# Kernel tuning notes

Hardware: AMD Instinct MI355X
Metric: run time of the kernel (lower is better)

## Reference

```python
import jax, jax.numpy as jnp
import numpy as np

H = 128            # hidden_channels
HM = 2 * H         # _inner_mlp_mult * H
N = 50000          # num nodes
E = 400000         # num edges
M = 800000         # num node-edge incidences (2 per edge)
BN_EPS = 1e-5


def _bn_relu(x, g, b):
    # BatchNorm1d in training mode: population stats over the batch dim, then affine + ReLU
    m = x.mean(0)
    v = ((x - m) ** 2).mean(0)
    return jax.nn.relu((x - m) * jax.lax.rsqrt(v + BN_EPS) * g + b)


def setup_inputs() -> dict:
    key = jax.random.key(0)
    ks = jax.random.split(key, 12)
    node_rep = jax.random.normal(ks[0], (N, H), dtype=jnp.float32)
    edge_rep = jax.random.normal(ks[1], (E, H), dtype=jnp.float32)
    src = jax.random.randint(ks[2], (M,), 0, N, dtype=jnp.int32)
    dst = jax.random.randint(ks[3], (M,), 0, E, dtype=jnp.int32)
    node2edge_index = jnp.stack([src, dst], 0)

    def lin(k, fan_in, fan_out):
        return jax.random.normal(k, (fan_in, fan_out), dtype=jnp.float32) / np.sqrt(fan_in)

    return {
        "node_rep": node_rep,
        "edge_rep": edge_rep,
        "node2edge_index": node2edge_index,
        # lvl_mlp_1: Linear(2H->H, no bias), BN(H), ReLU
        "Wa": lin(ks[4], 2 * H, H), "ga": jnp.ones((H,)), "ba": jnp.zeros((H,)),
        # lvl_mlp_2: Linear(H->2H), BN, ReLU, Linear(2H->H), BN, ReLU
        "Wb1": lin(ks[5], H, HM), "gb1": jnp.ones((HM,)), "bb1": jnp.zeros((HM,)),
        "Wb2": lin(ks[6], HM, H), "gb2": jnp.ones((H,)), "bb2": jnp.zeros((H,)),
        # lift_mlp: Linear(H->2H), BN, ReLU, Linear(2H->H), BN, ReLU
        "Wl1": lin(ks[7], H, HM), "gl1": jnp.ones((HM,)), "bl1": jnp.zeros((HM,)),
        "Wl2": lin(ks[8], HM, H), "gl2": jnp.ones((H,)), "bl2": jnp.zeros((H,)),
        "eps1": jnp.zeros(()), "eps2": jnp.zeros(()),
    }


def reference(node_rep, edge_rep, node2edge_index,
              Wa, ga, ba,
              Wb1, gb1, bb1, Wb2, gb2, bb2,
              Wl1, gl1, bl1, Wl2, gl2, bl2,
              eps1, eps2):
    src = node2edge_index[0]  # node index per incidence
    dst = node2edge_index[1]  # edge index per incidence

    # node -> edge gather + scatter_sum
    node2edge_val = node_rep[src]                                   # [M, H]
    lift_aggr = jax.ops.segment_sum(node2edge_val, dst, num_segments=E)  # [E, H]

    # lvl_mlp_1 on concatenated edge features
    lvl_aggr_edge = _bn_relu(jnp.concatenate([lift_aggr, edge_rep], -1) @ Wa, ga, ba)  # [E, H]

    # edge -> node gather + scatter_sum
    lvl_aggr = jax.ops.segment_sum(lvl_aggr_edge[dst], src, num_segments=N)  # [N, H]

    # lvl_mlp_2
    hn = (1.0 + eps1) * node_rep + lvl_aggr
    node_out = _bn_relu(_bn_relu(hn @ Wb1, gb1, bb1) @ Wb2, gb2, bb2)

    # lift_mlp
    he = (1.0 + eps2) * edge_rep + lift_aggr
    edge_out = _bn_relu(_bn_relu(he @ Wl1, gl1, bl1) @ Wl2, gl2, bl2)

    return node_out, edge_out
```

## Files before the change

### kernel.cpp

```cpp
#include <hip/hip_runtime.h>
#include <cstdint>
#include <cstddef>


typedef __bf16 bf16_t;
typedef __bf16 bf16x4 __attribute__((ext_vector_type(4)));
typedef __bf16 bf16x8 __attribute__((ext_vector_type(8)));
typedef float f32x4 __attribute__((ext_vector_type(4)));

__device__ __forceinline__ void atomAddF(float* p, float v) {
  unsafeAtomicAdd(p, v);
}

__device__ __forceinline__ void gload16(const void* g, void* l) {
  __builtin_amdgcn_global_load_lds(
      (const __attribute__((address_space(1))) unsigned int*)g,
      (__attribute__((address_space(3))) unsigned int*)l, 16, 0, 0);
}

template <int N>
__device__ __forceinline__ void waitVmC() {
  asm volatile("s_waitcnt vmcnt(%0)" ::"i"(N) : "memory");
}


__global__ __launch_bounds__(256) void k_hist(
    const int* __restrict__ src, const int* __restrict__ dst, int M,
    int* __restrict__ cnt_e, int* __restrict__ cnt_n) {
  int i = blockIdx.x * blockDim.x + threadIdx.x;
  if (i >= M) return;
  atomicAdd(cnt_e + dst[i], 1);
  atomicAdd(cnt_n + src[i], 1);
}

__global__ __launch_bounds__(256) void k_scan_block(
    const int* __restrict__ in, int* __restrict__ out, int* __restrict__ bsum,
    int L) {
  __shared__ int sh[256];
  int t = threadIdx.x;
  int base = (blockIdx.x * 256 + t) * 4;
  int v[4];
#pragma unroll
  for (int j = 0; j < 4; ++j) v[j] = (base + j < L) ? in[base + j] : 0;
  int tsum = v[0] + v[1] + v[2] + v[3];
  sh[t] = tsum;
  __syncthreads();
#pragma unroll
  for (int off = 1; off < 256; off <<= 1) {
    int x = (t >= off) ? sh[t - off] : 0;
    __syncthreads();
    sh[t] += x;
    __syncthreads();
  }
  int excl = sh[t] - tsum;
  if (t == 255) bsum[blockIdx.x] = sh[255];
  int run = excl;
#pragma unroll
  for (int j = 0; j < 4; ++j) {
    if (base + j < L) out[base + j] = run;
    run += v[j];
  }
}

__global__ __launch_bounds__(1024) void k_scan_top(int* __restrict__ bsum,
                                                   int nb) {
  __shared__ int sh[1024];
  __shared__ int running;
  int t = threadIdx.x;
  if (t == 0) running = 0;
  __syncthreads();
  for (int c = 0; c < nb; c += 1024) {
    int i = c + t;
    int v = (i < nb) ? bsum[i] : 0;
    sh[t] = v;
    __syncthreads();
#pragma unroll
    for (int off = 1; off < 1024; off <<= 1) {
      int x = (t >= off) ? sh[t - off] : 0;
      __syncthreads();
      sh[t] += x;
      __syncthreads();
    }
    int r = running;
    if (i < nb) bsum[i] = r + sh[t] - v;
    __syncthreads();
    if (t == 1023) running = r + sh[1023];
    __syncthreads();
  }
}

__global__ __launch_bounds__(256) void k_scan_add(int* __restrict__ out,
                                                  const int* __restrict__ bsum,
                                                  int L) {
  int base = (blockIdx.x * 256 + threadIdx.x) * 4;
  int add = bsum[blockIdx.x];
#pragma unroll
  for (int j = 0; j < 4; ++j)
    if (base + j < L) out[base + j] += add;
}

__global__ void k_settail(int* off_e, int E, int* off_n, int N, int M) {
  off_e[E] = M;
  off_n[N] = M;
}

__global__ __launch_bounds__(256) void k_fill(
    const int* __restrict__ src, const int* __restrict__ dst, int M,
    const int* __restrict__ off_e, int* __restrict__ fill_e,
    int* __restrict__ csr_e, const int* __restrict__ off_n,
    int* __restrict__ fill_n, int* __restrict__ csr_n) {
  int i = blockIdx.x * blockDim.x + threadIdx.x;
  if (i >= M) return;
  int s = src[i], d = dst[i];
  int pe = off_e[d] + atomicAdd(fill_e + d, 1);
  csr_e[pe] = s;
  int pn = off_n[s] + atomicAdd(fill_n + s, 1);
  csr_n[pn] = d;
}

__global__ __launch_bounds__(256) void k_wconv(const float* __restrict__ W,
                                               bf16_t* __restrict__ Wt, int K,
                                               int NC) {
  int idx = blockIdx.x * blockDim.x + threadIdx.x;
  if (idx >= K * NC) return;
  int k = idx / NC, n = idx % NC;
  Wt[(size_t)n * K + k] = (bf16_t)W[idx];
}

__global__ __launch_bounds__(256) void k_gather1(
    const float* __restrict__ node, const int* __restrict__ off_e,
    const int* __restrict__ csr_e, bf16_t* __restrict__ lift, int E) {
  int e = blockIdx.x * 8 + (threadIdx.x >> 5);
  if (e >= E) return;
  int l = threadIdx.x & 31;
  int b = off_e[e], en = off_e[e + 1];
  float4 acc = make_float4(0.f, 0.f, 0.f, 0.f);
  for (int j = b; j < en; ++j) {
    int r = csr_e[j];
    float4 v = *(const float4*)(node + (size_t)r * 128 + l * 4);
    acc.x += v.x; acc.y += v.y; acc.z += v.z; acc.w += v.w;
  }
  bf16x4 o;
  o[0] = (bf16_t)acc.x; o[1] = (bf16_t)acc.y;
  o[2] = (bf16_t)acc.z; o[3] = (bf16_t)acc.w;
  *(bf16x4*)(lift + (size_t)e * 128 + l * 4) = o;
}

__global__ __launch_bounds__(256) void k_gather2(
    const bf16_t* __restrict__ Y1, const float* __restrict__ st,
    const float* __restrict__ node, const int* __restrict__ off_n,
    const int* __restrict__ csr_n, const float* __restrict__ eps1p,
    bf16_t* __restrict__ hn, int N) {
  int n = blockIdx.x * 16 + (threadIdx.x >> 4);
  if (n >= N) return;
  int l = threadIdx.x & 15;
  float a1 = 1.0f + eps1p[0];
  float4 s0 = *(const float4*)(st + l * 8);
  float4 s1 = *(const float4*)(st + l * 8 + 4);
  float4 t0 = *(const float4*)(st + 128 + l * 8);
  float4 t1 = *(const float4*)(st + 128 + l * 8 + 4);
  float acc[8] = {0.f, 0.f, 0.f, 0.f, 0.f, 0.f, 0.f, 0.f};
  int b = off_n[n], en = off_n[n + 1];
  for (int j = b; j < en; ++j) {
    int r = csr_n[j];
    bf16x8 y = *(const bf16x8*)(Y1 + (size_t)r * 128 + l * 8);
    acc[0] += fmaxf(fmaf((float)y[0], s0.x, t0.x), 0.f);
    acc[1] += fmaxf(fmaf((float)y[1], s0.y, t0.y), 0.f);
    acc[2] += fmaxf(fmaf((float)y[2], s0.z, t0.z), 0.f);
    acc[3] += fmaxf(fmaf((float)y[3], s0.w, t0.w), 0.f);
    acc[4] += fmaxf(fmaf((float)y[4], s1.x, t1.x), 0.f);
    acc[5] += fmaxf(fmaf((float)y[5], s1.y, t1.y), 0.f);
    acc[6] += fmaxf(fmaf((float)y[6], s1.z, t1.z), 0.f);
    acc[7] += fmaxf(fmaf((float)y[7], s1.w, t1.w), 0.f);
  }
  float4 n0 = *(const float4*)(node + (size_t)n * 128 + l * 8);
  float4 n1 = *(const float4*)(node + (size_t)n * 128 + l * 8 + 4);
  bf16x8 hb;
  hb[0] = (bf16_t)fmaf(a1, n0.x, acc[0]);
  hb[1] = (bf16_t)fmaf(a1, n0.y, acc[1]);
  hb[2] = (bf16_t)fmaf(a1, n0.z, acc[2]);
  hb[3] = (bf16_t)fmaf(a1, n0.w, acc[3]);
  hb[4] = (bf16_t)fmaf(a1, n1.x, acc[4]);
  hb[5] = (bf16_t)fmaf(a1, n1.y, acc[5]);
  hb[6] = (bf16_t)fmaf(a1, n1.z, acc[6]);
  hb[7] = (bf16_t)fmaf(a1, n1.w, acc[7]);
  *(bf16x8*)(hn + (size_t)n * 128 + l * 8) = hb;
}


__global__ void k_bnfin(const float* __restrict__ sums, int C, int R,
                        const float* __restrict__ g, const float* __restrict__ b,
                        float* __restrict__ st) {
  int c = blockIdx.x * blockDim.x + threadIdx.x;
  if (c >= C) return;
  float invR = 1.f / (float)R;
  float mean = sums[c] * invR;
  float var = fmaxf(sums[C + c] * invR - mean * mean, 0.f);
  float s = g[c] * rsqrtf(var + 1e-5f);
  st[c] = s;
  st[C + c] = fmaf(-mean, s, b[c]);
}

__global__ __launch_bounds__(256) void k_bnrelu_out(
    const bf16_t* __restrict__ Y, const float* __restrict__ st, long R,
    float* __restrict__ out) {
  long t = (long)blockIdx.x * blockDim.x + threadIdx.x;
  long idx = t * 8;
  if (idx >= R * 128) return;
  int c = (int)(idx & 127);
  bf16x8 y = *(const bf16x8*)(Y + idx);
  float4 s0 = *(const float4*)(st + c);
  float4 s1 = *(const float4*)(st + c + 4);
  float4 t0 = *(const float4*)(st + 128 + c);
  float4 t1 = *(const float4*)(st + 128 + c + 4);
  float4 o0, o1;
  o0.x = fmaxf(fmaf((float)y[0], s0.x, t0.x), 0.f);
  o0.y = fmaxf(fmaf((float)y[1], s0.y, t0.y), 0.f);
  o0.z = fmaxf(fmaf((float)y[2], s0.z, t0.z), 0.f);
  o0.w = fmaxf(fmaf((float)y[3], s0.w, t0.w), 0.f);
  o1.x = fmaxf(fmaf((float)y[4], s1.x, t1.x), 0.f);
  o1.y = fmaxf(fmaf((float)y[5], s1.y, t1.y), 0.f);
  o1.z = fmaxf(fmaf((float)y[6], s1.z, t1.z), 0.f);
  o1.w = fmaxf(fmaf((float)y[7], s1.w, t1.w), 0.f);
  *(float4*)(out + idx) = o0;
  *(float4*)(out + idx + 4) = o1;
}

template <int K, int NC, int TRANSFORM>
__global__ __launch_bounds__(256, 3) void k_gemm_rb(
    const bf16_t* __restrict__ A, const bf16_t* __restrict__ Wt,
    const float* __restrict__ st, float* __restrict__ gstats,
    bf16_t* __restrict__ Y, int R) {
  constexpr int K2 = K * 2;
  constexpr int KF = K / 32;
  constexpr int CTW = NC / 64;
  constexpr int TR = 32;
  constexpr int RG = TR / 16;
  constexpr int TILEB = TR * K2;
  constexpr int WROWS = TR / 4;
  constexpr int STG = WROWS * K2 / 1024;
  constexpr int WCB = (NC / 4) * 2;
  constexpr int PATCH = TR * WCB;
  constexpr int CPR = WCB / 16;
  constexpr int RPP = 64 / CPR;
  constexpr int NPE = TR / RPP;
  constexpr int SWM = (WCB == 128) ? 7 : 3;
  constexpr int BTOT = NC * K2;
  constexpr int REG = 3 * TILEB;
  constexpr int NPASS = (BTOT + REG - 1) / REG;
  constexpr int WFULL = 2 * NPE + STG;
  constexpr int WTAIL = 2 * NPE;
  __shared__ __align__(16) char ldsc[3 * TILEB + 4 * PATCH + 2 * K * 4];
  const int tid = threadIdx.x;
  const int wv = tid >> 6, lane = tid & 63, quad = lane >> 4, l16 = lane & 15;

  if constexpr (TRANSFORM != 0) {
    for (int q = tid; q < 2 * K; q += 256)
      ((float*)(ldsc + 3 * TILEB + 4 * PATCH))[q] = st[q];
  }

  bf16x8 breg[CTW][KF];
  const char* Wtb = (const char*)Wt;
#pragma unroll
  for (int p = 0; p < NPASS; ++p) {
    const int base = p * REG;
    const int lim = (base + REG < BTOT) ? base + REG : BTOT;
    for (int q = base + tid * 16; q < lim; q += 4096)
      *(float4*)(ldsc + (q - base)) = *(const float4*)(Wtb + q);
    __syncthreads();
#pragma unroll
    for (int ct = 0; ct < CTW; ++ct) {
#pragma unroll
      for (int f = 0; f < KF; ++f) {
        const int bo =
            (wv * (NC / 4) + ct * 16 + l16) * K2 + f * 64 + quad * 16;
        if (bo >= base && bo < lim)
          breg[ct][f] = *(const bf16x8*)(ldsc + (bo - base));
      }
    }
    __syncthreads();
  }

  int stg_off[STG], stg_row[STG];
#pragma unroll
  for (int j = 0; j < STG; ++j) {
    const int p = j * 1024 + lane * 16;
    const int rl = p / K2;
    const int cg = ((p & (K2 - 1)) >> 4) ^ (rl & 7);
    stg_row[j] = rl;
    stg_off[j] = rl * K2 + cg * 16;
  }
  const int ntiles = (R + TR - 1) / TR;
  const int G = gridDim.x;
  auto stage = [&](int t, int b) {
    char* db = ldsc + b * TILEB + wv * (WROWS * K2);
    if (t * TR + TR <= R) {
      const char* srcb = (const char*)A + (size_t)(t * TR + wv * WROWS) * K2;
#pragma unroll
      for (int j = 0; j < STG; ++j) gload16(srcb + stg_off[j], db + j * 1024);
    } else {
#pragma unroll
      for (int j = 0; j < STG; ++j) {
        int g = t * TR + wv * WROWS + stg_row[j];
        if (g > R - 1) g = R - 1;
        gload16((const char*)A + (size_t)g * K2 +
                    (stg_off[j] - stg_row[j] * K2),
                db + j * 1024);
      }
    }
  };

  f32x4 csum4[CTW] = {}, csq4[CTW] = {};
  const float* sB = (const float*)(ldsc + 3 * TILEB + 4 * PATCH);
  char* patch = ldsc + 3 * TILEB + wv * PATCH;

  int t = blockIdx.x;
  if (t < ntiles) stage(t, 0);
  if (t + G < ntiles) stage(t + G, 1);
  waitVmC<STG>();
  __builtin_amdgcn_s_barrier();
  int c = 0;
  for (; t < ntiles; t += G) {
    const int t2 = t + 2 * G;
    const int b2 = (c >= 1) ? c - 1 : c + 2;
    if (t2 < ntiles) stage(t2, b2);

    const char* Ab = ldsc + c * TILEB;
    f32x4 acc[RG][CTW] = {};
#pragma unroll
    for (int f = 0; f < KF; ++f) {
      const int csw = ((f * 4 + quad) ^ (l16 & 7)) * 16;
      float4 s0, s1, u0, u1;
      if constexpr (TRANSFORM != 0) {
        const int k = f * 32 + quad * 8;
        s0 = *(const float4*)(sB + k);
        s1 = *(const float4*)(sB + k + 4);
        u0 = *(const float4*)(sB + K + k);
        u1 = *(const float4*)(sB + K + k + 4);
      }
#pragma unroll
      for (int rg = 0; rg < RG; ++rg) {
        bf16x8 a = *(const bf16x8*)(Ab + (rg * 16 + l16) * K2 + csw);
        if constexpr (TRANSFORM != 0) {
          bf16x8 o;
          o[0] = (bf16_t)fmaxf(fmaf((float)a[0], s0.x, u0.x), 0.f);
          o[1] = (bf16_t)fmaxf(fmaf((float)a[1], s0.y, u0.y), 0.f);
          o[2] = (bf16_t)fmaxf(fmaf((float)a[2], s0.z, u0.z), 0.f);
          o[3] = (bf16_t)fmaxf(fmaf((float)a[3], s0.w, u0.w), 0.f);
          o[4] = (bf16_t)fmaxf(fmaf((float)a[4], s1.x, u1.x), 0.f);
          o[5] = (bf16_t)fmaxf(fmaf((float)a[5], s1.y, u1.y), 0.f);
          o[6] = (bf16_t)fmaxf(fmaf((float)a[6], s1.z, u1.z), 0.f);
          o[7] = (bf16_t)fmaxf(fmaf((float)a[7], s1.w, u1.w), 0.f);
          a = o;
        }
#pragma unroll
        for (int ct = 0; ct < CTW; ++ct)
          acc[rg][ct] = __builtin_amdgcn_mfma_f32_16x16x32_bf16(
              breg[ct][f], a, acc[rg][ct], 0, 0, 0);
      }
    }
#pragma unroll
    for (int rg = 0; rg < RG; ++rg) {
      const int rl = rg * 16 + l16;
      const bool rok = (t * TR + rl) < R;
#pragma unroll
      for (int ct = 0; ct < CTW; ++ct) {
        const f32x4 v = acc[rg][ct];
        if (rok) {
          csum4[ct] += v;
          csq4[ct] += v * v;
        }
        bf16x4 pv;
        pv[0] = (bf16_t)v[0]; pv[1] = (bf16_t)v[1];
        pv[2] = (bf16_t)v[2]; pv[3] = (bf16_t)v[3];
        *(bf16x4*)(patch + rl * WCB +
                   ((ct * 32 + quad * 8) ^ ((rl & SWM) << 4))) = pv;
      }
    }
#pragma unroll
    for (int j = 0; j < NPE; ++j) {
      const int rl = j * RPP + lane / CPR;
      const int ch = lane & (CPR - 1);
      bf16x8 o =
          *(const bf16x8*)(patch + rl * WCB + ((ch * 16) ^ ((rl & SWM) << 4)));
      const int rowg = t * TR + rl;
      if (rowg < R)
        *(bf16x8*)((char*)Y + (size_t)rowg * (NC * 2) + wv * WCB + ch * 16) =
            o;
    }
    if (t2 < ntiles)
      waitVmC<WFULL>();
    else
      waitVmC<WTAIL>();
    __builtin_amdgcn_s_barrier();
    c = (c < 2) ? c + 1 : 0;
  }
#pragma unroll
  for (int ct = 0; ct < CTW; ++ct) {
    f32x4 s = csum4[ct], q = csq4[ct];
#pragma unroll
    for (int w = 1; w < 16; w <<= 1) {
#pragma unroll
      for (int r = 0; r < 4; ++r) {
        s[r] += __shfl_xor(s[r], w, 64);
        q[r] += __shfl_xor(q[r], w, 64);
      }
    }
    if (l16 == 0) {
      const int colb = wv * (NC / 4) + ct * 16 + quad * 4;
#pragma unroll
      for (int r = 0; r < 4; ++r) {
        atomAddF(gstats + colb + r, s[r]);
        atomAddF(gstats + NC + colb + r, q[r]);
      }
    }
  }
}

__global__ __launch_bounds__(256, 2) void k_gemm_cat_rb(
    const bf16_t* __restrict__ lift, const float* __restrict__ edge,
    const bf16_t* __restrict__ Wt, const float* __restrict__ eps2p,
    float* __restrict__ gstats, bf16_t* __restrict__ Y,
    bf16_t* __restrict__ he, int R) {
  constexpr int KF = 8, CTW = 2;
  __shared__ __align__(16) char ldsc[65536];
  const int tid = threadIdx.x;
  for (int p = tid * 16; p < 65536; p += 4096)
    *(float4*)(ldsc + p) = *(const float4*)((const char*)Wt + p);
  __syncthreads();
  const int wv = tid >> 6, lane = tid & 63, quad = lane >> 4, l16 = lane & 15;
  bf16x8 breg[CTW][KF];
#pragma unroll
  for (int ct = 0; ct < CTW; ++ct) {
    const int col = wv * 32 + ct * 16 + l16;
#pragma unroll
    for (int f = 0; f < KF; ++f)
      breg[ct][f] = *(const bf16x8*)(ldsc + col * 512 + f * 64 + quad * 16);
  }
  __syncthreads();

  const float a2 = 1.0f + eps2p[0];
  const int hi = lane >> 5;
  const int c32 = lane & 31;
  const int ntiles = (R + 63) >> 6;
  float4 ereg[8];
  bf16x4 lreg[8];
  auto loadRegs = [&](int t) {
#pragma unroll
    for (int it = 0; it < 8; ++it) {
      int g = t * 64 + wv * 16 + it * 2 + hi;
      if (g > R - 1) g = R - 1;
      ereg[it] = *(const float4*)(edge + (size_t)g * 128 + c32 * 4);
      lreg[it] = *(const bf16x4*)(lift + (size_t)g * 128 + c32 * 4);
    }
  };
  auto stageHe = [&](int t, int b) {
    char* db = ldsc + b * 32768;
#pragma unroll
    for (int it = 0; it < 8; ++it) {
      const int rl = wv * 16 + it * 2 + hi;
      const int g = t * 64 + rl;
      const float4 e = ereg[it];
      const bf16x4 lv = lreg[it];
      bf16x4 ev, hv;
      ev[0] = (bf16_t)e.x; ev[1] = (bf16_t)e.y;
      ev[2] = (bf16_t)e.z; ev[3] = (bf16_t)e.w;
      hv[0] = (bf16_t)fmaf(a2, e.x, (float)lv[0]);
      hv[1] = (bf16_t)fmaf(a2, e.y, (float)lv[1]);
      hv[2] = (bf16_t)fmaf(a2, e.z, (float)lv[2]);
      hv[3] = (bf16_t)fmaf(a2, e.w, (float)lv[3]);
      if (g < R) *(bf16x4*)(he + (size_t)g * 128 + c32 * 4) = hv;
      const int half = (c32 & 1) * 8;
      const int swl = (((c32 >> 1)) ^ (rl & 7)) * 16 + half;
      const int swe = (((c32 >> 1) + 16) ^ (rl & 7)) * 16 + half;
      *(bf16x4*)(db + rl * 512 + swl) = lv;
      *(bf16x4*)(db + rl * 512 + swe) = ev;
    }
  };

  f32x4 csum4[CTW] = {}, csq4[CTW] = {};
  int t = blockIdx.x, b = 0;
  if (t < ntiles) {
    loadRegs(t);
    stageHe(t, 0);
  }
  __syncthreads();
  for (; t < ntiles; t += gridDim.x) {
    const int tn = t + gridDim.x;
    if (tn < ntiles) loadRegs(tn);
    const char* Ab = ldsc + b * 32768;
    f32x4 acc[4][CTW] = {};
#pragma unroll
    for (int f = 0; f < KF; ++f) {
      const int csw = ((f * 4 + quad) ^ (l16 & 7)) * 16;
#pragma unroll
      for (int rg = 0; rg < 4; ++rg) {
        bf16x8 a = *(const bf16x8*)(Ab + (rg * 16 + l16) * 512 + csw);
#pragma unroll
        for (int ct = 0; ct < CTW; ++ct)
          acc[rg][ct] = __builtin_amdgcn_mfma_f32_16x16x32_bf16(
              breg[ct][f], a, acc[rg][ct], 0, 0, 0);
      }
    }
    __syncthreads();
    char* patch = ldsc + b * 32768 + wv * 8192;
#pragma unroll
    for (int rg = 0; rg < 4; ++rg) {
      const int rl = rg * 16 + l16;
      const bool rok = (t * 64 + rl) < R;
#pragma unroll
      for (int ct = 0; ct < CTW; ++ct) {
        const f32x4 v = acc[rg][ct];
        if (rok) {
          csum4[ct] += v;
          csq4[ct] += v * v;
        }
        bf16x4 pv;
        pv[0] = (bf16_t)v[0]; pv[1] = (bf16_t)v[1];
        pv[2] = (bf16_t)v[2]; pv[3] = (bf16_t)v[3];
        *(bf16x4*)(patch + rl * 64 + ((ct * 32 + quad * 8) ^ ((rl & 3) << 4))) =
            pv;
      }
    }
#pragma unroll
    for (int j = 0; j < 4; ++j) {
      const int rl = j * 16 + (lane >> 2);
      const int ch = lane & 3;
      bf16x8 o = *(const bf16x8*)(patch + rl * 64 + ((ch * 16) ^ ((rl & 3) << 4)));
      const int rowg = t * 64 + rl;
      if (rowg < R)
        *(bf16x8*)((char*)Y + (size_t)rowg * 256 + wv * 64 + ch * 16) = o;
    }
    if (tn < ntiles) stageHe(tn, b ^ 1);
    __syncthreads();
    b ^= 1;
  }
#pragma unroll
  for (int ct = 0; ct < CTW; ++ct) {
    f32x4 s = csum4[ct], q = csq4[ct];
#pragma unroll
    for (int w = 1; w < 16; w <<= 1) {
#pragma unroll
      for (int r = 0; r < 4; ++r) {
        s[r] += __shfl_xor(s[r], w, 64);
        q[r] += __shfl_xor(q[r], w, 64);
      }
    }
    if (l16 == 0) {
      const int colb = wv * 32 + ct * 16 + quad * 4;
#pragma unroll
      for (int r = 0; r < 4; ++r) {
        atomAddF(gstats + colb + r, s[r]);
        atomAddF(gstats + 128 + colb + r, q[r]);
      }
    }
  }
}


extern "C" void kernel_launch(void* const* d_in, const int* in_sizes, int n_in,
                              void* d_out, int out_size, void* d_ws,
                              size_t ws_size, hipStream_t stream) {
  const float* node_rep = (const float*)d_in[0];
  const float* edge_rep = (const float*)d_in[1];
  const int* n2e = (const int*)d_in[2];
  const float* Wa = (const float*)d_in[3];
  const float* ga = (const float*)d_in[4];
  const float* ba = (const float*)d_in[5];
  const float* Wb1 = (const float*)d_in[6];
  const float* gb1 = (const float*)d_in[7];
  const float* bb1 = (const float*)d_in[8];
  const float* Wb2 = (const float*)d_in[9];
  const float* gb2 = (const float*)d_in[10];
  const float* bb2 = (const float*)d_in[11];
  const float* Wl1 = (const float*)d_in[12];
  const float* gl1 = (const float*)d_in[13];
  const float* bl1 = (const float*)d_in[14];
  const float* Wl2 = (const float*)d_in[15];
  const float* gl2 = (const float*)d_in[16];
  const float* bl2 = (const float*)d_in[17];
  const float* eps1 = (const float*)d_in[18];
  const float* eps2 = (const float*)d_in[19];

  const int N = in_sizes[0] / 128;
  const int E = in_sizes[1] / 128;
  const int M = in_sizes[2] / 2;
  const int* srcI = n2e;
  const int* dstI = n2e + M;

  char* wsb = (char*)d_ws;
  size_t off = 0;
  auto alloc = [&](size_t bytes) {
    void* p = wsb + off;
    off += (bytes + 255) & ~(size_t)255;
    return p;
  };
  bf16_t* lift = (bf16_t*)alloc((size_t)E * 128 * 2);
  bf16_t* he   = (bf16_t*)alloc((size_t)E * 128 * 2);
  bf16_t* Y1   = (bf16_t*)alloc((size_t)E * 128 * 2);
  bf16_t* Ze   = (bf16_t*)alloc((size_t)E * 256 * 2);
  bf16_t* Y2e  = (bf16_t*)alloc((size_t)E * 128 * 2);
  bf16_t* hn   = (bf16_t*)alloc((size_t)N * 128 * 2);
  bf16_t* Zn   = (bf16_t*)alloc((size_t)N * 256 * 2);
  bf16_t* Y2n  = (bf16_t*)alloc((size_t)N * 128 * 2);
  bf16_t* Wa_t  = (bf16_t*)alloc(256 * 128 * 2);
  bf16_t* Wb1_t = (bf16_t*)alloc(128 * 256 * 2);
  bf16_t* Wb2_t = (bf16_t*)alloc(256 * 128 * 2);
  bf16_t* Wl1_t = (bf16_t*)alloc(128 * 256 * 2);
  bf16_t* Wl2_t = (bf16_t*)alloc(256 * 128 * 2);
  int* zbase  = (int*)alloc(((size_t)E * 2 + (size_t)N * 2 + 8192) * 4);
  int* cnt_e  = zbase;
  int* fill_e = zbase + E;
  int* cnt_n  = zbase + 2 * (size_t)E;
  int* fill_n = zbase + 2 * (size_t)E + N;
  float* stats = (float*)(zbase + 2 * (size_t)E + 2 * (size_t)N);
  int* off_e  = (int*)alloc((size_t)(E + 1) * 4);
  int* csr_e  = (int*)alloc((size_t)M * 4);
  int* off_n  = (int*)alloc((size_t)(N + 1) * 4);
  int* csr_n  = (int*)alloc((size_t)M * 4);
  int* bsumE  = (int*)alloc(4096 * 4);
  int* bsumN  = (int*)alloc(4096 * 4);

  float* sum_a  = stats + 0;
  float* st_a   = stats + 256;
  float* sum_b1 = stats + 512;
  float* st_b1  = stats + 1024;
  float* sum_b2 = stats + 1536;
  float* st_b2  = stats + 1792;
  float* sum_l1 = stats + 2048;
  float* st_l1  = stats + 2560;
  float* sum_l2 = stats + 3072;
  float* st_l2  = stats + 3328;

  float* node_out = (float*)d_out;
  float* edge_out = (float*)d_out + (size_t)N * 128;

  hipMemsetAsync(zbase, 0, ((size_t)E * 2 + (size_t)N * 2 + 8192) * 4, stream);

  k_hist<<<(M + 255) / 256, 256, 0, stream>>>(srcI, dstI, M, cnt_e, cnt_n);
  const int nbE = (E + 1023) / 1024;
  const int nbN = (N + 1023) / 1024;
  k_scan_block<<<nbE, 256, 0, stream>>>(cnt_e, off_e, bsumE, E);
  k_scan_top<<<1, 1024, 0, stream>>>(bsumE, nbE);
  k_scan_add<<<nbE, 256, 0, stream>>>(off_e, bsumE, E);
  k_scan_block<<<nbN, 256, 0, stream>>>(cnt_n, off_n, bsumN, N);
  k_scan_top<<<1, 1024, 0, stream>>>(bsumN, nbN);
  k_scan_add<<<nbN, 256, 0, stream>>>(off_n, bsumN, N);
  k_settail<<<1, 1, 0, stream>>>(off_e, E, off_n, N, M);
  k_fill<<<(M + 255) / 256, 256, 0, stream>>>(srcI, dstI, M, off_e, fill_e,
                                              csr_e, off_n, fill_n, csr_n);

  k_wconv<<<128, 256, 0, stream>>>(Wa, Wa_t, 256, 128);
  k_wconv<<<128, 256, 0, stream>>>(Wb1, Wb1_t, 128, 256);
  k_wconv<<<128, 256, 0, stream>>>(Wb2, Wb2_t, 256, 128);
  k_wconv<<<128, 256, 0, stream>>>(Wl1, Wl1_t, 128, 256);
  k_wconv<<<128, 256, 0, stream>>>(Wl2, Wl2_t, 256, 128);

  const int ntE = (E + 31) / 32, gE = ntE < 768 ? ntE : 768;
  const int ntN = (N + 31) / 32, gN = ntN < 768 ? ntN : 768;
  const int ntEc = (E + 63) / 64, gEc = ntEc < 512 ? ntEc : 512;

  k_gather1<<<(E + 7) / 8, 256, 0, stream>>>(node_rep, off_e, csr_e, lift, E);

  k_gemm_cat_rb<<<gEc, 256, 0, stream>>>(lift, edge_rep, Wa_t, eps2, sum_a,
                                         Y1, he, E);
  k_bnfin<<<1, 256, 0, stream>>>(sum_a, 128, E, ga, ba, st_a);

  k_gather2<<<(N + 15) / 16, 256, 0, stream>>>(Y1, st_a, node_rep, off_n,
                                               csr_n, eps1, hn, N);

  k_gemm_rb<128, 256, 0><<<gN, 256, 0, stream>>>(hn, Wb1_t, nullptr, sum_b1,
                                                 Zn, N);
  k_bnfin<<<1, 256, 0, stream>>>(sum_b1, 256, N, gb1, bb1, st_b1);
  k_gemm_rb<256, 128, 1><<<gN, 256, 0, stream>>>(Zn, Wb2_t, st_b1, sum_b2,
                                                 Y2n, N);
  k_bnfin<<<1, 256, 0, stream>>>(sum_b2, 128, N, gb2, bb2, st_b2);
  {
    long total = ((long)N * 128 + 7) / 8;
    k_bnrelu_out<<<(int)((total + 255) / 256), 256, 0, stream>>>(Y2n, st_b2, N,
                                                                 node_out);
  }

  k_gemm_rb<128, 256, 0><<<gE, 256, 0, stream>>>(he, Wl1_t, nullptr, sum_l1,
                                                 Ze, E);
  k_bnfin<<<1, 256, 0, stream>>>(sum_l1, 256, E, gl1, bl1, st_l1);
  k_gemm_rb<256, 128, 1><<<gE, 256, 0, stream>>>(Ze, Wl2_t, st_l1, sum_l2,
                                                 Y2e, E);
  k_bnfin<<<1, 256, 0, stream>>>(sum_l2, 128, E, gl2, bl2, st_l2);
  {
    long total = ((long)E * 128 + 7) / 8;
    k_bnrelu_out<<<(int)((total + 255) / 256), 256, 0, stream>>>(Y2e, st_l2, E,
                                                                 edge_out);
  }
}
```

Before: 1.334 ms.

## Replace block-shared GEMM pipeline with per-wave private LDS staging and no barriers

The row-block GEMM is rewritten so each wave owns its own LDS region, stages 16-row tiles with direct global-to-LDS loads, and double-buffers them (by tile or by K half) without block-wide barriers. Weights are loaded straight from global into registers instead of through shared LDS passes. Occupancy is raised to 4 blocks per CU and grids to 1024 blocks. This removes s_barrier stalls and the weight-staging syncs, but each wave now reloads and processes the full A tile redundantly across waves, which increases A traffic.

Result: slower. 1.519 ms (+13.8%).

```diff
diff --git a/kernel.cpp b/kernel.cpp
--- a/kernel.cpp
+++ b/kernel.cpp
@@ -21,6 +21,9 @@
 template <int N>
 __device__ __forceinline__ void waitVmC() {
   asm volatile("s_waitcnt vmcnt(%0)" ::"i"(N) : "memory");
+}
+__device__ __forceinline__ void waitLgkm0() {
+  asm volatile("s_waitcnt lgkmcnt(0)" ::: "memory");
 }
 
 
@@ -227,191 +230,187 @@
 }
 
 template <int K, int NC, int TRANSFORM>
-__global__ __launch_bounds__(256, 3) void k_gemm_rb(
+__global__ __launch_bounds__(256, 4) void k_gemm_wd(
     const bf16_t* __restrict__ A, const bf16_t* __restrict__ Wt,
     const float* __restrict__ st, float* __restrict__ gstats,
     bf16_t* __restrict__ Y, int R) {
   constexpr int K2 = K * 2;
-  constexpr int KF = K / 32;
+  constexpr int NCH = K / 128;
   constexpr int CTW = NC / 64;
-  constexpr int TR = 32;
-  constexpr int RG = TR / 16;
-  constexpr int TILEB = TR * K2;
-  constexpr int WROWS = TR / 4;
-  constexpr int STG = WROWS * K2 / 1024;
   constexpr int WCB = (NC / 4) * 2;
-  constexpr int PATCH = TR * WCB;
+  constexpr int SWM = WCB / 16 - 1;
   constexpr int CPR = WCB / 16;
   constexpr int RPP = 64 / CPR;
-  constexpr int NPE = TR / RPP;
-  constexpr int SWM = (WCB == 128) ? 7 : 3;
-  constexpr int BTOT = NC * K2;
-  constexpr int REG = 3 * TILEB;
-  constexpr int NPASS = (BTOT + REG - 1) / REG;
-  constexpr int WFULL = 2 * NPE + STG;
-  constexpr int WTAIL = 2 * NPE;
-  __shared__ __align__(16) char ldsc[3 * TILEB + 4 * PATCH + 2 * K * 4];
+  constexpr int NST = 16 / RPP;
+  constexpr int WVB = 8192 + (TRANSFORM ? 2048 : 0);
+  __shared__ __align__(16) char lds[4 * WVB];
   const int tid = threadIdx.x;
   const int wv = tid >> 6, lane = tid & 63, quad = lane >> 4, l16 = lane & 15;
-
+  char* wb = lds + wv * WVB;
+  float* stw = (float*)(wb + 8192);
   if constexpr (TRANSFORM != 0) {
-    for (int q = tid; q < 2 * K; q += 256)
-      ((float*)(ldsc + 3 * TILEB + 4 * PATCH))[q] = st[q];
-  }
-
-  bf16x8 breg[CTW][KF];
-  const char* Wtb = (const char*)Wt;
-#pragma unroll
-  for (int p = 0; p < NPASS; ++p) {
-    const int base = p * REG;
-    const int lim = (base + REG < BTOT) ? base + REG : BTOT;
-    for (int q = base + tid * 16; q < lim; q += 4096)
-      *(float4*)(ldsc + (q - base)) = *(const float4*)(Wtb + q);
-    __syncthreads();
+#pragma unroll
+    for (int i = 0; i < 8; ++i) stw[lane + i * 64] = st[lane + i * 64];
+  }
+  const int sc0 = wv * (NC / 4);
+  bf16x8 breg[CTW][NCH * 4];
+#pragma unroll
+  for (int ct = 0; ct < CTW; ++ct)
+#pragma unroll
+    for (int f = 0; f < NCH * 4; ++f)
+      breg[ct][f] = *(const bf16x8*)((const char*)Wt +
+                                     (size_t)(sc0 + ct * 16 + l16) * K2 +
+                                     f * 64 + quad * 16);
+  int srow[4], scg[4];
+#pragma unroll
+  for (int j = 0; j < 4; ++j) {
+    const int p = j * 1024 + lane * 16;
+    srow[j] = p >> 8;
+    scg[j] = (((p & 255) >> 4) ^ (srow[j] & 7)) << 4;
+  }
+  const int nt = (R + 15) >> 4;
+  const int G = gridDim.x;
+  const char* Ab = (const char*)A;
+  auto stage = [&](int r, int h, int slot) {
+    char* db = wb + slot * 4096;
+#pragma unroll
+    for (int j = 0; j < 4; ++j) {
+      int g = r * 16 + srow[j];
+      if (g > R - 1) g = R - 1;
+      gload16(Ab + (size_t)g * K2 + h * 256 + scg[j], db + j * 1024);
+    }
+  };
+  f32x4 csum[CTW] = {}, csq[CTW] = {};
+  auto computeChunk = [&](int h, int slot, f32x4* acc) {
+    const char* cb = wb + slot * 4096;
+#pragma unroll
+    for (int fl = 0; fl < 4; ++fl) {
+      const int f = h * 4 + fl;
+      bf16x8 a = *(const bf16x8*)(cb + l16 * 256 +
+                                  (((fl * 4 + quad) ^ (l16 & 7)) << 4));
+      if constexpr (TRANSFORM != 0) {
+        const int k0 = f * 32 + quad * 8;
+        const float4 s0 = *(const float4*)(stw + k0);
+        const float4 s1 = *(const float4*)(stw + k0 + 4);
+        const float4 u0 = *(const float4*)(stw + K + k0);
+        const float4 u1 = *(const float4*)(stw + K + k0 + 4);
+        bf16x8 o;
+        o[0] = (bf16_t)fmaxf(fmaf((float)a[0], s0.x, u0.x), 0.f);
+        o[1] = (bf16_t)fmaxf(fmaf((float)a[1], s0.y, u0.y), 0.f);
+        o[2] = (bf16_t)fmaxf(fmaf((float)a[2], s0.z, u0.z), 0.f);
+        o[3] = (bf16_t)fmaxf(fmaf((float)a[3], s0.w, u0.w), 0.f);
+        o[4] = (bf16_t)fmaxf(fmaf((float)a[4], s1.x, u1.x), 0.f);
+        o[5] = (bf16_t)fmaxf(fmaf((float)a[5], s1.y, u1.y), 0.f);
+        o[6] = (bf16_t)fmaxf(fmaf((float)a[6], s1.z, u1.z), 0.f);
+        o[7] = (bf16_t)fmaxf(fmaf((float)a[7], s1.w, u1.w), 0.f);
+        a = o;
+      }
+#pragma unroll
+      for (int ct = 0; ct < CTW; ++ct)
+        acc[ct] = __builtin_amdgcn_mfma_f32_16x16x32_bf16(breg[ct][f], a,
+                                                          acc[ct], 0, 0, 0);
+    }
+  };
+  auto epilogue = [&](int r, int slot, f32x4* acc) {
+    char* patch = wb + slot * 4096;
+    const bool rok = (r * 16 + l16) < R;
 #pragma unroll
     for (int ct = 0; ct < CTW; ++ct) {
-#pragma unroll
-      for (int f = 0; f < KF; ++f) {
-        const int bo =
-            (wv * (NC / 4) + ct * 16 + l16) * K2 + f * 64 + quad * 16;
-        if (bo >= base && bo < lim)
-          breg[ct][f] = *(const bf16x8*)(ldsc + (bo - base));
-      }
-    }
-    __syncthreads();
-  }
-
-  int stg_off[STG], stg_row[STG];
-#pragma unroll
-  for (int j = 0; j < STG; ++j) {
-    const int p = j * 1024 + lane * 16;
-    const int rl = p / K2;
-    const int cg = ((p & (K2 - 1)) >> 4) ^ (rl & 7);
-    stg_row[j] = rl;
-    stg_off[j] = rl * K2 + cg * 16;
-  }
-  const int ntiles = (R + TR - 1) / TR;
-  const int G = gridDim.x;
-  auto stage = [&](int t, int b) {
-    char* db = ldsc + b * TILEB + wv * (WROWS * K2);
-    if (t * TR + TR <= R) {
-      const char* srcb = (const char*)A + (size_t)(t * TR + wv * WROWS) * K2;
-#pragma unroll
-      for (int j = 0; j < STG; ++j) gload16(srcb + stg_off[j], db + j * 1024);
+      const f32x4 v = acc[ct];
+      if (rok) {
+        csum[ct] += v;
+        csq[ct] += v * v;
+      }
+      bf16x4 pv;
+      pv[0] = (bf16_t)v[0]; pv[1] = (bf16_t)v[1];
+      pv[2] = (bf16_t)v[2]; pv[3] = (bf16_t)v[3];
+      const int c16 = ct * 2 + (quad >> 1);
+      *(bf16x4*)(patch + l16 * WCB + (((c16 ^ (l16 & SWM)) << 4)) +
+                 (quad & 1) * 8) = pv;
+    }
+    waitLgkm0();
+    __builtin_amdgcn_sched_barrier(0);
+#pragma unroll
+    for (int ps = 0; ps < NST; ++ps) {
+      const int rl = ps * RPP + lane / CPR;
+      const int c16 = lane & (CPR - 1);
+      bf16x8 o =
+          *(const bf16x8*)(patch + rl * WCB + ((c16 ^ (rl & SWM)) << 4));
+      const int row = r * 16 + rl;
+      if (row < R)
+        *(bf16x8*)((char*)Y + (size_t)row * (NC * 2) + wv * WCB + c16 * 16) =
+            o;
+    }
+  };
+
+  const int r0 = blockIdx.x;
+  if constexpr (NCH == 1) {
+    stage(r0, 0, 0);
+    if (r0 + G < nt) {
+      stage(r0 + G, 0, 1);
+      waitVmC<4>();
     } else {
-#pragma unroll
-      for (int j = 0; j < STG; ++j) {
-        int g = t * TR + wv * WROWS + stg_row[j];
-        if (g > R - 1) g = R - 1;
-        gload16((const char*)A + (size_t)g * K2 +
-                    (stg_off[j] - stg_row[j] * K2),
-                db + j * 1024);
-      }
-    }
-  };
-
-  f32x4 csum4[CTW] = {}, csq4[CTW] = {};
-  const float* sB = (const float*)(ldsc + 3 * TILEB + 4 * PATCH);
-  char* patch = ldsc + 3 * TILEB + wv * PATCH;
-
-  int t = blockIdx.x;
-  if (t < ntiles) stage(t, 0);
-  if (t + G < ntiles) stage(t + G, 1);
-  waitVmC<STG>();
-  __builtin_amdgcn_s_barrier();
-  int c = 0;
-  for (; t < ntiles; t += G) {
-    const int t2 = t + 2 * G;
-    const int b2 = (c >= 1) ? c - 1 : c + 2;
-    if (t2 < ntiles) stage(t2, b2);
-
-    const char* Ab = ldsc + c * TILEB;
-    f32x4 acc[RG][CTW] = {};
-#pragma unroll
-    for (int f = 0; f < KF; ++f) {
-      const int csw = ((f * 4 + quad) ^ (l16 & 7)) * 16;
-      float4 s0, s1, u0, u1;
-      if constexpr (TRANSFORM != 0) {
-        const int k = f * 32 + quad * 8;
-        s0 = *(const float4*)(sB + k);
-        s1 = *(const float4*)(sB + k + 4);
-        u0 = *(const float4*)(sB + K + k);
-        u1 = *(const float4*)(sB + K + k + 4);
-      }
-#pragma unroll
-      for (int rg = 0; rg < RG; ++rg) {
-        bf16x8 a = *(const bf16x8*)(Ab + (rg * 16 + l16) * K2 + csw);
-        if constexpr (TRANSFORM != 0) {
-          bf16x8 o;
-          o[0] = (bf16_t)fmaxf(fmaf((float)a[0], s0.x, u0.x), 0.f);
-          o[1] = (bf16_t)fmaxf(fmaf((float)a[1], s0.y, u0.y), 0.f);
-          o[2] = (bf16_t)fmaxf(fmaf((float)a[2], s0.z, u0.z), 0.f);
-          o[3] = (bf16_t)fmaxf(fmaf((float)a[3], s0.w, u0.w), 0.f);
-          o[4] = (bf16_t)fmaxf(fmaf((float)a[4], s1.x, u1.x), 0.f);
-          o[5] = (bf16_t)fmaxf(fmaf((float)a[5], s1.y, u1.y), 0.f);
-          o[6] = (bf16_t)fmaxf(fmaf((float)a[6], s1.z, u1.z), 0.f);
-          o[7] = (bf16_t)fmaxf(fmaf((float)a[7], s1.w, u1.w), 0.f);
-          a = o;
-        }
-#pragma unroll
-        for (int ct = 0; ct < CTW; ++ct)
-          acc[rg][ct] = __builtin_amdgcn_mfma_f32_16x16x32_bf16(
-              breg[ct][f], a, acc[rg][ct], 0, 0, 0);
-      }
-    }
-#pragma unroll
-    for (int rg = 0; rg < RG; ++rg) {
-      const int rl = rg * 16 + l16;
-      const bool rok = (t * TR + rl) < R;
-#pragma unroll
-      for (int ct = 0; ct < CTW; ++ct) {
-        const f32x4 v = acc[rg][ct];
-        if (rok) {
-          csum4[ct] += v;
-          csq4[ct] += v * v;
-        }
-        bf16x4 pv;
-        pv[0] = (bf16_t)v[0]; pv[1] = (bf16_t)v[1];
-        pv[2] = (bf16_t)v[2]; pv[3] = (bf16_t)v[3];
-        *(bf16x4*)(patch + rl * WCB +
-                   ((ct * 32 + quad * 8) ^ ((rl & SWM) << 4))) = pv;
-      }
-    }
-#pragma unroll
-    for (int j = 0; j < NPE; ++j) {
-      const int rl = j * RPP + lane / CPR;
-      const int ch = lane & (CPR - 1);
-      bf16x8 o =
-          *(const bf16x8*)(patch + rl * WCB + ((ch * 16) ^ ((rl & SWM) << 4)));
-      const int rowg = t * TR + rl;
-      if (rowg < R)
-        *(bf16x8*)((char*)Y + (size_t)rowg * (NC * 2) + wv * WCB + ch * 16) =
-            o;
-    }
-    if (t2 < ntiles)
-      waitVmC<WFULL>();
-    else
-      waitVmC<WTAIL>();
-    __builtin_amdgcn_s_barrier();
-    c = (c < 2) ? c + 1 : 0;
+      waitVmC<0>();
+    }
+    __builtin_amdgcn_sched_barrier(0);
+    int i = 0;
+    for (int t = r0; t < nt; t += G, ++i) {
+      const int slot = i & 1;
+      f32x4 acc[CTW] = {};
+      computeChunk(0, slot, acc);
+      epilogue(t, slot, acc);
+      if (t + 2 * G < nt) {
+        stage(t + 2 * G, 0, slot);
+        waitVmC<NST + 4>();
+      } else {
+        waitVmC<NST>();
+      }
+      __builtin_amdgcn_sched_barrier(0);
+    }
+  } else {
+    stage(r0, 0, 0);
+    stage(r0, 1, 1);
+    waitVmC<4>();
+    __builtin_amdgcn_sched_barrier(0);
+    for (int t = r0; t < nt; t += G) {
+      f32x4 acc[CTW] = {};
+      computeChunk(0, 0, acc);
+      const bool more = (t + G < nt);
+      if (more) {
+        stage(t + G, 0, 0);
+        waitVmC<4>();
+      } else {
+        waitVmC<0>();
+      }
+      __builtin_amdgcn_sched_barrier(0);
+      computeChunk(1, 1, acc);
+      epilogue(t, 1, acc);
+      if (more) {
+        stage(t + G, 1, 1);
+        waitVmC<NST + 4>();
+      } else {
+        waitVmC<0>();
+      }
+      __builtin_amdgcn_sched_barrier(0);
+    }
   }
 #pragma unroll
   for (int ct = 0; ct < CTW; ++ct) {
-    f32x4 s = csum4[ct], q = csq4[ct];
+    f32x4 s = csum[ct], q = csq[ct];
 #pragma unroll
     for (int w = 1; w < 16; w <<= 1) {
 #pragma unroll
-      for (int r = 0; r < 4; ++r) {
-        s[r] += __shfl_xor(s[r], w, 64);
-        q[r] += __shfl_xor(q[r], w, 64);
+      for (int rr = 0; rr < 4; ++rr) {
+        s[rr] += __shfl_xor(s[rr], w, 64);
+        q[rr] += __shfl_xor(q[rr], w, 64);
       }
     }
     if (l16 == 0) {
-      const int colb = wv * (NC / 4) + ct * 16 + quad * 4;
-#pragma unroll
-      for (int r = 0; r < 4; ++r) {
-        atomAddF(gstats + colb + r, s[r]);
-        atomAddF(gstats + NC + colb + r, q[r]);
+      const int colb = sc0 + ct * 16 + quad * 4;
+#pragma unroll
+      for (int rr = 0; rr < 4; ++rr) {
+        atomAddF(gstats + colb + rr, s[rr]);
+        atomAddF(gstats + NC + colb + rr, q[rr]);
       }
     }
   }
@@ -526,7 +525,8 @@
     for (int j = 0; j < 4; ++j) {
       const int rl = j * 16 + (lane >> 2);
       const int ch = lane & 3;
-      bf16x8 o = *(const bf16x8*)(patch + rl * 64 + ((ch * 16) ^ ((rl & 3) << 4)));
+      bf16x8 o =
+          *(const bf16x8*)(patch + rl * 64 + ((ch * 16) ^ ((rl & 3) << 4)));
       const int rowg = t * 64 + rl;
       if (rowg < R)
         *(bf16x8*)((char*)Y + (size_t)rowg * 256 + wv * 64 + ch * 16) = o;
@@ -656,9 +656,9 @@
   k_wconv<<<128, 256, 0, stream>>>(Wl1, Wl1_t, 128, 256);
   k_wconv<<<128, 256, 0, stream>>>(Wl2, Wl2_t, 256, 128);
 
-  const int ntE = (E + 31) / 32, gE = ntE < 768 ? ntE : 768;
-  const int ntN = (N + 31) / 32, gN = ntN < 768 ? ntN : 768;
   const int ntEc = (E + 63) / 64, gEc = ntEc < 512 ? ntEc : 512;
+  const int ntN16 = (N + 15) / 16, gNw = ntN16 < 1024 ? ntN16 : 1024;
+  const int ntE16 = (E + 15) / 16, gEw = ntE16 < 1024 ? ntE16 : 1024;
 
   k_gather1<<<(E + 7) / 8, 256, 0, stream>>>(node_rep, off_e, csr_e, lift, E);
 
@@ -669,11 +669,11 @@
   k_gather2<<<(N + 15) / 16, 256, 0, stream>>>(Y1, st_a, node_rep, off_n,
                                                csr_n, eps1, hn, N);
 
-  k_gemm_rb<128, 256, 0><<<gN, 256, 0, stream>>>(hn, Wb1_t, nullptr, sum_b1,
-                                                 Zn, N);
+  k_gemm_wd<128, 256, 0><<<gNw, 256, 0, stream>>>(hn, Wb1_t, nullptr, sum_b1,
+                                                  Zn, N);
   k_bnfin<<<1, 256, 0, stream>>>(sum_b1, 256, N, gb1, bb1, st_b1);
-  k_gemm_rb<256, 128, 1><<<gN, 256, 0, stream>>>(Zn, Wb2_t, st_b1, sum_b2,
-                                                 Y2n, N);
+  k_gemm_wd<256, 128, 1><<<gNw, 256, 0, stream>>>(Zn, Wb2_t, st_b1, sum_b2,
+                                                  Y2n, N);
   k_bnfin<<<1, 256, 0, stream>>>(sum_b2, 128, N, gb2, bb2, st_b2);
   {
     long total = ((long)N * 128 + 7) / 8;
@@ -681,11 +681,11 @@
                                                                  node_out);
   }
 
-  k_gemm_rb<128, 256, 0><<<gE, 256, 0, stream>>>(he, Wl1_t, nullptr, sum_l1,
-                                                 Ze, E);
+  k_gemm_wd<128, 256, 0><<<gEw, 256, 0, stream>>>(he, Wl1_t, nullptr, sum_l1,
+                                                  Ze, E);
   k_bnfin<<<1, 256, 0, stream>>>(sum_l1, 256, E, gl1, bl1, st_l1);
-  k_gemm_rb<256, 128, 1><<<gE, 256, 0, stream>>>(Ze, Wl2_t, st_l1, sum_l2,
-                                                 Y2e, E);
+  k_gemm_wd<256, 128, 1><<<gEw, 256, 0, stream>>>(Ze, Wl2_t, st_l1, sum_l2,
+                                                  Y2e, E);
   k_bnfin<<<1, 256, 0, stream>>>(sum_l2, 128, E, gl2, bl2, st_l2);
   {
     long total = ((long)E * 128 + 7) / 8;
```
